# Optimization experiments

Hardware: AMD Instinct MI355X
Metric: run time of the kernel (lower is better)

## Reference

```python
import jax, jax.numpy as jnp
import numpy as np

KNOTS = 17  # integration points on [0, 3]


def _buffers():
    t = jnp.linspace(0.0, 3.0, KNOTS, dtype=jnp.float32)
    dt = 3.0 / (KNOTS - 1)
    w = jnp.full((KNOTS,), 2.0 * dt, dtype=jnp.float32)
    w = w.at[0].set(dt).at[-1].set(dt)          # trapezoid-style end weights
    phi = jnp.exp(-jnp.square(t) / 2.0)         # ideal Gaussian ECF
    return t, phi, w * phi


def setup_inputs() -> dict:
    key = jax.random.key(0)
    k1, k2 = jax.random.split(key)
    N, D, P = 8192, 512, 1024
    z = jax.random.normal(k1, (N, D), dtype=jnp.float32)
    A = jax.random.normal(k2, (D, P), dtype=jnp.float32)  # random projections (hoisted from forward)
    return {"z": z, "A": A}


def reference(z, A):
    t, phi, weights = _buffers()
    D = z.shape[-1]
    flat = z.reshape(-1, D).astype(jnp.float32)            # [N, D]
    An = A / jnp.clip(jnp.linalg.norm(A, axis=0, keepdims=True), 1e-8)
    proj = flat @ An                                       # [N, P]
    x_t = proj[:, :, None] * t                             # [N, P, K]
    cos_mean = jnp.mean(jnp.cos(x_t), axis=0)              # [P, K]
    sin_mean = jnp.mean(jnp.sin(x_t), axis=0)              # [P, K]
    err = jnp.square(cos_mean - phi) + jnp.square(sin_mean)
    statistic = (err @ weights) * flat.shape[0]            # [P]
    return jnp.mean(statistic)
```

## Files before the change

### kernel.cpp

```cpp
#include <hip/hip_runtime.h>
#include <stdint.h>

#define N_SAMP 8192
#define D_DIM  512
#define P_DIM  1024
#define DT     0.1875f

typedef float f32x4 __attribute__((ext_vector_type(4)));
typedef float f32x2 __attribute__((ext_vector_type(2)));
typedef short bf16x8 __attribute__((ext_vector_type(8)));
typedef unsigned short u16;

__device__ __forceinline__ u16 f2bf(float x){
    unsigned int u = __float_as_uint(x);
    return (u16)((u + 0x7FFFu + ((u >> 16) & 1u)) >> 16);
}

__device__ __forceinline__ void load_lds16(const void* g, void* l){
    __builtin_amdgcn_global_load_lds(
        (const __attribute__((address_space(1))) void*)(uintptr_t)g,
        (__attribute__((address_space(3))) void*)(uint32_t)(uintptr_t)l,
        16, 0, 0);
}

__global__ __launch_bounds__(256) void k_prep(const float4* __restrict__ z4,
                                              u16* __restrict__ zb,
                                              const float* __restrict__ A,
                                              float* __restrict__ inv,
                                              u16* __restrict__ AnT,
                                              float* __restrict__ gpart,
                                              float* __restrict__ out){
    const int tid = threadIdx.x;
    const int b = blockIdx.x;
    if (b < 4096){
        int i = b * 256 + tid;
        if (i == 0) out[0] = 0.f;
        float4 v = z4[i];
        ushort4 o;
        o.x = f2bf(v.x); o.y = f2bf(v.y); o.z = f2bf(v.z); o.w = f2bf(v.w);
        ((ushort4*)zb)[i] = o;
        return;
    }
    if (b < 4128){
        __shared__ float red[8][32];
        const int p0 = (b - 4096) * 32;
        const int pl = tid & 31, dg = tid >> 5;
        float s = 0.f;
        #pragma unroll 8
        for (int i = 0; i < 64; ++i){
            float v = A[(size_t)(dg + 8 * i) * P_DIM + p0 + pl];
            s += v * v;
        }
        red[dg][pl] = s;
        __syncthreads();
        if (tid < 32){
            float t = 0.f;
            #pragma unroll
            for (int g = 0; g < 8; ++g) t += red[g][tid];
            inv[p0 + tid] = 1.0f / fmaxf(sqrtf(t), 1e-8f);
        }
        return;
    }
    if (b < 4640){
        __shared__ float tile[32][33];
        const int t = b - 4128;
        const int p0 = (t & 31) * 32, d0 = (t >> 5) * 32;
        const int tx = tid & 31, ty = tid >> 5;
        #pragma unroll
        for (int j = 0; j < 4; ++j)
            tile[ty + j * 8][tx] = A[(size_t)(d0 + ty + j * 8) * P_DIM + p0 + tx];
        __syncthreads();
        #pragma unroll
        for (int j = 0; j < 4; ++j){
            int pp = ty + j * 8;
            AnT[(size_t)(p0 + pp) * D_DIM + d0 + tx] = f2bf(tile[tx][pp]);
        }
        return;
    }
    int i = (b - 4640) * 256 + tid;
    ((float4*)gpart)[i] = (float4){0.f, 0.f, 0.f, 0.f};
}

__global__ __launch_bounds__(512) void k_gemm_ecf(const u16* __restrict__ zb,
                                                  const u16* __restrict__ AnT,
                                                  const float* __restrict__ inv,
                                                  float* __restrict__ gpart){
    __shared__ uint4 smem4[4096];
    const int tid = threadIdx.x;
    const int swz = (blockIdx.x & 7) * 64 + (blockIdx.x >> 3);
    const int bm = swz >> 3, bn = swz & 7;
    const int m0 = bm << 7, n0 = bn << 7;
    const int w = tid >> 6, lane = tid & 63;
    const int r = lane & 15, kg = lane >> 4;
    const int wm = (w >> 2) << 6;
    const int wn = (w & 3) << 5;

    const int srow = tid >> 3;
    const int gsw  = ((tid & 7) ^ (srow & 7)) << 3;
    const u16* gA = zb  + (size_t)(m0 + srow) * D_DIM + gsw;
    const u16* gB = AnT + (size_t)(n0 + srow) * D_DIM + gsw;
    char* lbase = (char*)smem4 + w * 1024;

    f32x4 acc[4][2] = {};

    #pragma unroll
    for (int h = 0; h < 2; ++h){
        load_lds16(gA + (size_t)h * 64 * D_DIM, lbase + h * 8192);
        load_lds16(gB + (size_t)h * 64 * D_DIM, lbase + 16384 + h * 8192);
    }

    for (int kt = 0; kt < 8; ++kt){
        const int cur = kt & 1;
        __syncthreads();
        if (kt < 7){
            char* la = lbase + ((kt + 1) & 1) * 32768;
            #pragma unroll
            for (int h = 0; h < 2; ++h){
                load_lds16(gA + (size_t)h * 64 * D_DIM + (kt + 1) * 64, la + h * 8192);
                load_lds16(gB + (size_t)h * 64 * D_DIM + (kt + 1) * 64, la + 16384 + h * 8192);
            }
        }
        const u16* Ab = (const u16*)smem4 + cur * 16384;
        const u16* Bb = Ab + 8192;
        #pragma unroll
        for (int ks = 0; ks < 2; ++ks){
            bf16x8 af[4], bfr[2];
            #pragma unroll
            for (int i = 0; i < 4; ++i)
                af[i] = *(const bf16x8*)&Ab[(wm + i * 16 + r) * 64 +
                                            (((ks * 4 + kg) ^ (r & 7)) << 3)];
            #pragma unroll
            for (int j = 0; j < 2; ++j)
                bfr[j] = *(const bf16x8*)&Bb[(wn + j * 16 + r) * 64 +
                                             (((ks * 4 + kg) ^ (r & 7)) << 3)];
            #pragma unroll
            for (int i = 0; i < 4; ++i)
                #pragma unroll
                for (int j = 0; j < 2; ++j)
                    acc[i][j] = __builtin_amdgcn_mfma_f32_16x16x32_bf16(
                        af[i], bfr[j], acc[i][j], 0, 0, 0);
        }
    }

    __syncthreads();
    float* epil = (float*)smem4;
    #pragma unroll
    for (int jn = 0; jn < 2; ++jn){
        const float sc = inv[n0 + wn + jn * 16 + r] * DT;
        f32x2 sum[16];
        #pragma unroll
        for (int k = 0; k < 16; ++k) sum[k] = (f32x2){0.f, 0.f};
        #pragma unroll
        for (int i = 0; i < 4; ++i){
            #pragma unroll
            for (int q = 0; q < 4; ++q){
                float x = acc[i][jn][q] * sc;
                float s1, c1;
                __sincosf(x, &s1, &c1);
                float tc = c1 + c1;
                f32x2 prev = {1.f, 0.f};
                f32x2 curv = {c1, s1};
                sum[0] += curv;
                #pragma unroll
                for (int k = 2; k <= 16; ++k){
                    f32x2 nxt = tc * curv - prev;
                    sum[k - 1] += nxt;
                    prev = curv; curv = nxt;
                }
            }
        }
        #pragma unroll
        for (int k = 0; k < 16; ++k){
            f32x2 o;
            o.x = __shfl_xor(sum[k].x, 16); o.y = __shfl_xor(sum[k].y, 16);
            sum[k] += o;
            o.x = __shfl_xor(sum[k].x, 32); o.y = __shfl_xor(sum[k].y, 32);
            sum[k] += o;
        }
        if (lane < 16){
            const int cl = jn * 16 + lane;
            #pragma unroll
            for (int k = 0; k < 16; ++k){
                epil[(w * 32 + k)      * 32 + cl] = sum[k].x;
                epil[(w * 32 + 16 + k) * 32 + cl] = sum[k].y;
            }
        }
    }
    __syncthreads();
    for (int f0 = 0; f0 < 4096; f0 += 512){
        int f = f0 + tid;
        int cl = f & 127, j = f >> 7;
        int whi = cl >> 5, cll = cl & 31;
        float v = epil[((whi    ) * 32 + j) * 32 + cll] +
                  epil[((whi + 4) * 32 + j) * 32 + cll];
        atomicAdd(&gpart[j * P_DIM + n0 + cl], v);
    }
}

__global__ __launch_bounds__(256) void k_reduce(const float* __restrict__ gpart,
                                                float* __restrict__ out){
    const int tid = threadIdx.x;
    const int idx = blockIdx.x * 256 + tid;
    const int j = idx >> 10;
    float s = gpart[idx];
    const int k = (j & 15) + 1;
    float tk = (float)k * DT;
    float phik = expf(-0.5f * tk * tk);
    float wk = ((k == 16) ? DT : 2.f * DT) * phik;
    float mean = s * (1.f / (float)N_SAMP);
    float diff = (j < 16) ? (mean - phik) : mean;
    float term = diff * diff * wk;
    #pragma unroll
    for (int o = 32; o > 0; o >>= 1) term += __shfl_xor(term, o);
    __shared__ float red[4];
    if ((tid & 63) == 0) red[tid >> 6] = term;
    __syncthreads();
    if (tid == 0)
        atomicAdd(out, (red[0] + red[1] + red[2] + red[3]) *
                       ((float)N_SAMP / (float)P_DIM));
}

extern "C" void kernel_launch(void* const* d_in, const int* in_sizes, int n_in,
                              void* d_out, int out_size, void* d_ws, size_t ws_size,
                              hipStream_t stream){
    const float* z = (const float*)d_in[0];
    const float* A = (const float*)d_in[1];
    char* ws = (char*)d_ws;
    float* inv   = (float*)(ws);
    float* gpart = (float*)(ws + 8192);
    u16*   AnT   = (u16*)  (ws + 139264);
    u16*   zb    = (u16*)  (ws + 1187840);
    float* out   = (float*)d_out;

    hipLaunchKernelGGL(k_prep,     dim3(4672), dim3(256), 0, stream,
                       (const float4*)z, zb, A, inv, AnT, gpart, out);
    hipLaunchKernelGGL(k_gemm_ecf, dim3(512),  dim3(512), 0, stream,
                       zb, AnT, inv, gpart);
    hipLaunchKernelGGL(k_reduce,   dim3(128),  dim3(256), 0, stream, gpart, out);
}
```

Baseline: 41.49 us.

## Load GEMM B fragments directly from global into registers, halving LDS footprint

```diff
diff --git a/kernel.cpp b/kernel.cpp
--- a/kernel.cpp
+++ b/kernel.cpp
@@ -81,11 +81,44 @@
     ((float4*)gpart)[i] = (float4){0.f, 0.f, 0.f, 0.f};
 }
 
+#define GEMM_ITER(KT, BC, BN)                                                  \
+  {                                                                            \
+    __syncthreads();                                                           \
+    if ((KT) < 7){                                                             \
+      _Pragma("unroll")                                                        \
+      for (int ks = 0; ks < 2; ++ks)                                           \
+        _Pragma("unroll")                                                      \
+        for (int j = 0; j < 2; ++j)                                            \
+          BN[ks][j] = *(const bf16x8*)&gB[(size_t)j * 16 * D_DIM +             \
+                                          ((KT) + 1) * 64 + ks * 32];          \
+      char* la = lbase + (((KT) + 1) & 1) * 16384;                             \
+      _Pragma("unroll")                                                        \
+      for (int h = 0; h < 2; ++h)                                              \
+        load_lds16(gA + (size_t)h * 64 * D_DIM + ((KT) + 1) * 64,              \
+                   la + h * 8192);                                             \
+    }                                                                          \
+    const u16* Ab = (const u16*)smem4 + ((KT) & 1) * 8192;                     \
+    _Pragma("unroll")                                                          \
+    for (int ks = 0; ks < 2; ++ks){                                            \
+      bf16x8 af[4];                                                            \
+      _Pragma("unroll")                                                        \
+      for (int i = 0; i < 4; ++i)                                              \
+        af[i] = *(const bf16x8*)&Ab[(wm + i * 16 + r) * 64 +                   \
+                                    (((ks * 4 + kg) ^ (r & 7)) << 3)];         \
+      _Pragma("unroll")                                                        \
+      for (int i = 0; i < 4; ++i)                                              \
+        _Pragma("unroll")                                                      \
+        for (int j = 0; j < 2; ++j)                                            \
+          acc[i][j] = __builtin_amdgcn_mfma_f32_16x16x32_bf16(                 \
+              af[i], BC[ks][j], acc[i][j], 0, 0, 0);                           \
+    }                                                                          \
+  }
+
 __global__ __launch_bounds__(512) void k_gemm_ecf(const u16* __restrict__ zb,
                                                   const u16* __restrict__ AnT,
                                                   const float* __restrict__ inv,
                                                   float* __restrict__ gpart){
-    __shared__ uint4 smem4[4096];
+    __shared__ uint4 smem4[2048];
     const int tid = threadIdx.x;
     const int swz = (blockIdx.x & 7) * 64 + (blockIdx.x >> 3);
     const int bm = swz >> 3, bn = swz & 7;
@@ -97,49 +130,26 @@
 
     const int srow = tid >> 3;
     const int gsw  = ((tid & 7) ^ (srow & 7)) << 3;
-    const u16* gA = zb  + (size_t)(m0 + srow) * D_DIM + gsw;
-    const u16* gB = AnT + (size_t)(n0 + srow) * D_DIM + gsw;
+    const u16* gA = zb + (size_t)(m0 + srow) * D_DIM + gsw;
     char* lbase = (char*)smem4 + w * 1024;
 
+    const u16* gB = AnT + (size_t)(n0 + wn + r) * D_DIM + kg * 8;
+
     f32x4 acc[4][2] = {};
-
-    #pragma unroll
-    for (int h = 0; h < 2; ++h){
+    bf16x8 bA[2][2], bB[2][2];
+
+    #pragma unroll
+    for (int h = 0; h < 2; ++h)
         load_lds16(gA + (size_t)h * 64 * D_DIM, lbase + h * 8192);
-        load_lds16(gB + (size_t)h * 64 * D_DIM, lbase + 16384 + h * 8192);
-    }
-
-    for (int kt = 0; kt < 8; ++kt){
-        const int cur = kt & 1;
-        __syncthreads();
-        if (kt < 7){
-            char* la = lbase + ((kt + 1) & 1) * 32768;
-            #pragma unroll
-            for (int h = 0; h < 2; ++h){
-                load_lds16(gA + (size_t)h * 64 * D_DIM + (kt + 1) * 64, la + h * 8192);
-                load_lds16(gB + (size_t)h * 64 * D_DIM + (kt + 1) * 64, la + 16384 + h * 8192);
-            }
-        }
-        const u16* Ab = (const u16*)smem4 + cur * 16384;
-        const u16* Bb = Ab + 8192;
-        #pragma unroll
-        for (int ks = 0; ks < 2; ++ks){
-            bf16x8 af[4], bfr[2];
-            #pragma unroll
-            for (int i = 0; i < 4; ++i)
-                af[i] = *(const bf16x8*)&Ab[(wm + i * 16 + r) * 64 +
-                                            (((ks * 4 + kg) ^ (r & 7)) << 3)];
-            #pragma unroll
-            for (int j = 0; j < 2; ++j)
-                bfr[j] = *(const bf16x8*)&Bb[(wn + j * 16 + r) * 64 +
-                                             (((ks * 4 + kg) ^ (r & 7)) << 3)];
-            #pragma unroll
-            for (int i = 0; i < 4; ++i)
-                #pragma unroll
-                for (int j = 0; j < 2; ++j)
-                    acc[i][j] = __builtin_amdgcn_mfma_f32_16x16x32_bf16(
-                        af[i], bfr[j], acc[i][j], 0, 0, 0);
-        }
+    #pragma unroll
+    for (int ks = 0; ks < 2; ++ks)
+        #pragma unroll
+        for (int j = 0; j < 2; ++j)
+            bA[ks][j] = *(const bf16x8*)&gB[(size_t)j * 16 * D_DIM + ks * 32];
+
+    for (int kt2 = 0; kt2 < 4; ++kt2){
+        GEMM_ITER(2 * kt2,     bA, bB);
+        GEMM_ITER(2 * kt2 + 1, bB, bA);
     }
 
     __syncthreads();
```

New measurement: 48.14 us. 1.16x slower.
